# Kernel optimization log

Measured on AMD Instinct MI355X. Metric: run time of the kernel, lower is better.

Reference implementation:

```python
import jax, jax.numpy as jnp
import numpy as np

ZERO_TOL = 1e-06
KSZ = 3


def setup_inputs() -> dict:
    key = jax.random.key(0)
    k1, k2, k3, k4 = jax.random.split(key, 4)
    B, C, H, W = 8, 3, 64, 64
    NC = 16
    D = 2 * C * KSZ * KSZ  # 54
    x = jax.random.normal(k1, (B, C, H, W), dtype=jnp.float32)
    mask = jax.random.uniform(k2, (NC, D), dtype=jnp.float32, minval=-1.0, maxval=1.0)
    weight = jax.random.uniform(k3, (NC, D), dtype=jnp.float32, minval=0.0, maxval=1.0)
    # module init: bias = mean over channels of weight.sum(1)/2 (constant per channel)
    bias = jnp.full((NC, 1), (weight.sum(1) / 2.0).mean(), dtype=jnp.float32)
    return {"x": x, "mask": mask, "weight": weight, "bias": bias}


def _wos_forward(x, mask, weight, bias):
    B, C, H, W = x.shape
    NC = weight.shape[0]
    # fixed_padding for kernel 3, dilation 1 -> pad 1 on each side ('same')
    xp = jnp.pad(x, ((0, 0), (0, 0), (1, 1), (1, 1)))
    # unfold: torch ordering flattens (C, kh, kw) with C slowest
    patches = jnp.stack(
        [xp[:, :, i:i + H, j:j + W] for i in range(KSZ) for j in range(KSZ)],
        axis=2,
    )  # (B, C, k*k, H, W)
    D0 = C * KSZ * KSZ
    L = H * W
    unf = patches.reshape(B, D0, L)                    # (B, D0, L) like nn.Unfold
    inp = jnp.transpose(unf, (0, 2, 1)).reshape(B * L, 1, D0)  # rows ordered b*L+l
    inp = jnp.concatenate([inp, -inp], axis=2)         # (N, 1, D)
    mx = inp + mask[None]                              # (N, NC, D)
    si = jnp.argsort(-mx, axis=-1)                     # descending sort permutation
    smx = jnp.take_along_axis(mx, si, axis=-1)         # sorted values, descending
    sw = jnp.take_along_axis(jnp.broadcast_to(weight[None], mx.shape), si, axis=-1)
    nz = sw > ZERO_TOL                                 # nonzero-weight positions
    # cumulative sum over the compacted (nonzero) weights, kept in full coords
    accw = jnp.cumsum(jnp.where(nz, sw, 0.0), axis=-1)
    li = jnp.sum(nz & (accw <= bias[None]), axis=-1) - 1   # (N, NC)
    li = jnp.maximum(li, 0)
    # rank among nonzero entries; pick the li-th nonzero sorted value
    rank = jnp.cumsum(nz.astype(jnp.int32), axis=-1) - 1
    sel = nz & (rank == li[..., None])
    y = jnp.sum(jnp.where(sel, smx, 0.0), axis=-1)     # (N, NC)
    # module does result.view(-1, NC, L_sqrt, L_sqrt): raw reinterpret of memory
    return y.reshape(B, NC, H, W)


def reference(x, mask, weight, bias):
    return _wos_forward(x, mask, weight, bias)
```

## Files before the change

kernel.cpp:

```cpp
#include <hip/hip_runtime.h>
#include <limits.h>
#include <math.h>
#include <stdint.h>

#define WOS_ZERO_TOL 1e-6f
#define STRIDE 57

__global__ __launch_bounds__(256) void wos_kernel(
    const float* __restrict__ x,
    const float* __restrict__ mask,
    const float* __restrict__ weight,
    const float* __restrict__ bias,
    float* __restrict__ out)
{
    __shared__ float s_ws[4][16][STRIDE];
    __shared__ float s_mx[4][16][STRIDE];
    __shared__ unsigned long long s_key[4][64];

    const int lane = threadIdx.x & 63;
    const int wid  = threadIdx.x >> 6;
    const int p    = blockIdx.x * 4 + wid;
    const int b    = p >> 12;
    const int l    = p & 4095;
    const int h    = l >> 6;
    const int w    = l & 63;

    float inp = 0.0f;
    if (lane < 54) {
        int dm  = (lane < 27) ? lane : lane - 27;
        int c   = dm / 9;
        int rem = dm - 9 * c;
        int di  = rem / 3;
        int dj  = rem - 3 * di;
        int hh  = h + di - 1;
        int ww  = w + dj - 1;
        if (hh >= 0 && hh < 64 && ww >= 0 && ww < 64) {
            float v = x[((b * 3 + c) << 12) + (hh << 6) + ww];
            inp = (lane < 27) ? v : -v;
        }
    }

    const uint32_t inv_lane = (uint32_t)(63 - lane);

    #pragma unroll 1
    for (int nc = 0; nc < 16; ++nc) {
        float mk   = (lane < 54) ? mask[nc * 54 + lane]   : 0.0f;
        float wv   = (lane < 54) ? weight[nc * 54 + lane] : 0.0f;
        float mxv  = (lane < 54) ? (inp + mk) : -INFINITY;
        float wsel = (wv > WOS_ZERO_TOL) ? wv : 0.0f;

        int      bits = __float_as_int(mxv);
        uint32_t ob   = (uint32_t)(bits ^ ((bits >> 31) | 0x80000000));
        uint64_t myk  = ((uint64_t)ob << 32) | inv_lane;

        s_key[wid][lane] = myk;

        uint32_t rank = 0;
        #pragma unroll
        for (int dp = 0; dp < 54; ++dp) {
            rank += (s_key[wid][dp] > myk) ? 1u : 0u;
        }

        if (lane < 54) {
            s_ws[wid][nc][rank] = wsel;
            s_mx[wid][nc][rank] = mxv;
        }
    }

    {
        const int   nc = lane & 15;
        const float bv = bias[nc];
        float acc   = 0.0f;
        int   rstar = -1;
        int   fnz   = 64;
        #pragma unroll
        for (int r = 0; r < 54; ++r) {
            float wr = s_ws[wid][nc][r];
            acc += wr;
            bool nz = (__float_as_int(wr) != 0);
            rstar = (nz && acc <= bv) ? r : rstar;
            fnz   = (nz && r < fnz)   ? r : fnz;
        }
        if (rstar < 0) rstar = (fnz < 54) ? fnz : 0;
        float ans = s_mx[wid][nc][rstar];
        if (lane < 16) out[p * 16 + lane] = ans;
    }
}

extern "C" void kernel_launch(void* const* d_in, const int* in_sizes, int n_in,
                              void* d_out, int out_size, void* d_ws, size_t ws_size,
                              hipStream_t stream) {
    const float* x      = (const float*)d_in[0];
    const float* mask   = (const float*)d_in[1];
    const float* weight = (const float*)d_in[2];
    const float* bias   = (const float*)d_in[3];
    float* out = (float*)d_out;

    wos_kernel<<<dim3(8192), dim3(256), 0, stream>>>(x, mask, weight, bias, out);
}
```

Before: 202.2 us.

## Halve shared memory with grouped channels, interleaved float2 storage and vectorized rank loads

Splits the 16 channels into two groups of 8 and resolves each group's selection before moving on, so the per-wave sorted buffer holds only 8 channels. Weight and value now sit together as a float2, which roughly halves LDS use per block, and launch_bounds now requests 8 blocks per CU for higher occupancy. The rank count reads keys two at a time as ulonglong2 to cut LDS load instructions. The selection pass now picks the value directly instead of an index, at the cost of an extra select pass and a second round of output writes per group.

```diff
diff --git a/kernel.cpp b/kernel.cpp
--- a/kernel.cpp
+++ b/kernel.cpp
@@ -6,15 +6,14 @@
 #define WOS_ZERO_TOL 1e-6f
 #define STRIDE 57
 
-__global__ __launch_bounds__(256) void wos_kernel(
+__global__ __launch_bounds__(256, 8) void wos_kernel(
     const float* __restrict__ x,
     const float* __restrict__ mask,
     const float* __restrict__ weight,
     const float* __restrict__ bias,
     float* __restrict__ out)
 {
-    __shared__ float s_ws[4][16][STRIDE];
-    __shared__ float s_mx[4][16][STRIDE];
+    __shared__ float2 s_wm[4][8][STRIDE];
     __shared__ unsigned long long s_key[4][64];
 
     const int lane = threadIdx.x & 63;
@@ -43,47 +42,53 @@
     const uint32_t inv_lane = (uint32_t)(63 - lane);
 
     #pragma unroll 1
-    for (int nc = 0; nc < 16; ++nc) {
-        float mk   = (lane < 54) ? mask[nc * 54 + lane]   : 0.0f;
-        float wv   = (lane < 54) ? weight[nc * 54 + lane] : 0.0f;
-        float mxv  = (lane < 54) ? (inp + mk) : -INFINITY;
-        float wsel = (wv > WOS_ZERO_TOL) ? wv : 0.0f;
+    for (int g = 0; g < 2; ++g) {
+        #pragma unroll 1
+        for (int i = 0; i < 8; ++i) {
+            const int nc = g * 8 + i;
+            float mk   = (lane < 54) ? mask[nc * 54 + lane]   : 0.0f;
+            float wv   = (lane < 54) ? weight[nc * 54 + lane] : 0.0f;
+            float mxv  = (lane < 54) ? (inp + mk) : -INFINITY;
+            float wsel = (wv > WOS_ZERO_TOL) ? wv : 0.0f;
 
-        int      bits = __float_as_int(mxv);
-        uint32_t ob   = (uint32_t)(bits ^ ((bits >> 31) | 0x80000000));
-        uint64_t myk  = ((uint64_t)ob << 32) | inv_lane;
+            int      bits = __float_as_int(mxv);
+            uint32_t ob   = (uint32_t)(bits ^ ((bits >> 31) | 0x80000000));
+            uint64_t myk  = ((uint64_t)ob << 32) | inv_lane;
 
-        s_key[wid][lane] = myk;
+            s_key[wid][lane] = myk;
 
-        uint32_t rank = 0;
-        #pragma unroll
-        for (int dp = 0; dp < 54; ++dp) {
-            rank += (s_key[wid][dp] > myk) ? 1u : 0u;
+            const ulonglong2* kp =
+                reinterpret_cast<const ulonglong2*>(&s_key[wid][0]);
+            uint32_t rank = 0;
+            #pragma unroll
+            for (int dp = 0; dp < 27; ++dp) {
+                ulonglong2 kk = kp[dp];
+                rank += (kk.x > myk) ? 1u : 0u;
+                rank += (kk.y > myk) ? 1u : 0u;
+            }
+
+            if (lane < 54) {
+                s_wm[wid][i][rank] = make_float2(wsel, mxv);
+            }
         }
 
-        if (lane < 54) {
-            s_ws[wid][nc][rank] = wsel;
-            s_mx[wid][nc][rank] = mxv;
+        {
+            const int   nc8 = lane & 7;
+            const float bv  = bias[g * 8 + nc8];
+            float acc   = 0.0f;
+            float ans   = 0.0f;
+            bool  found = false;
+            #pragma unroll
+            for (int r = 0; r < 54; ++r) {
+                float2 wm = s_wm[wid][nc8][r];
+                acc += wm.x;
+                bool nz   = (__float_as_int(wm.x) != 0);
+                bool take = nz && (acc <= bv || !found);
+                found     = found || nz;
+                ans       = take ? wm.y : ans;
+            }
+            if (lane < 8) out[p * 16 + g * 8 + lane] = ans;
         }
-    }
-
-    {
-        const int   nc = lane & 15;
-        const float bv = bias[nc];
-        float acc   = 0.0f;
-        int   rstar = -1;
-        int   fnz   = 64;
-        #pragma unroll
-        for (int r = 0; r < 54; ++r) {
-            float wr = s_ws[wid][nc][r];
-            acc += wr;
-            bool nz = (__float_as_int(wr) != 0);
-            rstar = (nz && acc <= bv) ? r : rstar;
-            fnz   = (nz && r < fnz)   ? r : fnz;
-        }
-        if (rstar < 0) rstar = (fnz < 54) ? fnz : 0;
-        float ans = s_mx[wid][nc][rstar];
-        if (lane < 16) out[p * 16 + lane] = ans;
     }
 }
 
```

After: 274.4 us. 1.36x slower.
